# Kernel optimization log

Hardware: AMD Instinct MI355X
Metric: run time of the kernel (lower is better)

Reference implementation:

```python
import jax, jax.numpy as jnp
import numpy as np

N = 100000   # vertices
T = 128      # temporal depth
E = 1600000  # edges (avg degree 16)
K = 9        # conv kernel size
PAD = 4      # 'same' padding -> T preserved
L = 3        # number of layers


def setup_inputs() -> dict:
    key = jax.random.key(0)
    ks = jax.random.split(key, 6)
    x = jax.random.normal(ks[0], (N, T), dtype=jnp.float32)
    edge_index = jax.random.randint(ks[1], (2, E), 0, N, dtype=jnp.int32)
    conv_w = jax.random.normal(ks[2], (L, 1, 1, K), dtype=jnp.float32) * (1.0 / np.sqrt(K))
    conv_b = jax.random.normal(ks[3], (L, 1), dtype=jnp.float32) * 0.1
    W_out = jax.random.normal(ks[4], (3, N), dtype=jnp.float32) * (1.0 / np.sqrt(N))
    b_out = jax.random.normal(ks[5], (3,), dtype=jnp.float32) * 0.1
    return {"x": x, "edge_index": edge_index, "conv_w": conv_w,
            "conv_b": conv_b, "W_out": W_out, "b_out": b_out}


def _conv1d(x, w, b):
    # x: [N, T], w: [1, 1, K] (OIH), b: [1]; torch Conv1d = cross-correlation.
    y = jax.lax.conv_general_dilated(
        x[:, None, :], w, window_strides=(1,), padding=[(PAD, PAD)],
        dimension_numbers=("NCH", "OIH", "NCH"))
    return y[:, 0, :] + b  # [N, T]


def reference(x, edge_index, conv_w, conv_b, W_out, b_out):
    # add_self_loops: append (i, i) for every node
    loop = jnp.arange(N, dtype=edge_index.dtype)
    src = jnp.concatenate([edge_index[0], loop])  # message sources
    dst = jnp.concatenate([edge_index[1], loop])  # aggregation targets
    # in-degree counts (>=1 due to self loops) for mean aggregation
    cnt = jax.ops.segment_sum(jnp.ones(src.shape, jnp.float32), dst,
                              num_segments=N)[:, None]  # [N, 1]
    for i in range(L):
        h = _conv1d(x, conv_w[i], conv_b[i])                    # [N, T]
        s = jax.ops.segment_sum(h[src], dst, num_segments=N)    # scatter-sum of gathered msgs
        x = jax.nn.relu(s / cnt)                                # mean aggr + relu
    x = x.reshape(-1, N)            # [T, N] (row-major view like torch .view)
    return x @ W_out.T + b_out      # [T, 3]
```

## Files before the change

### kernel.cpp

```cpp
#include <hip/hip_runtime.h>

#define NN 100000
#define TT 128
#define EE 1600000
#define KK 9
#define NSPLIT 16
#define ZROW NN

#define BSH 9
#define BMASK 511
#define NBUCK 196
#define BCAP 10240
#define EPB 4096
#define BINB 391
#define CVTB 3125

typedef _Float16 f16;
typedef __attribute__((ext_vector_type(2))) _Float16 f16x2;
typedef __attribute__((ext_vector_type(4))) _Float16 f16x4;
typedef __attribute__((ext_vector_type(8))) _Float16 f16x8;

union HU8 { f16x8 h; int4 i; };

__global__ __launch_bounds__(1024)
void bin_cvt_kernel(const int* __restrict__ ei, int* __restrict__ gcursor,
                    unsigned int* __restrict__ binned,
                    const float4* __restrict__ x, f16x4* __restrict__ x16,
                    float* __restrict__ out,
                    int* __restrict__ zx, int* __restrict__ zyA, int* __restrict__ zyB) {
    __shared__ int hist[NBUCK];
    __shared__ int gbase[NBUCK];
    int tid = threadIdx.x;

    if (blockIdx.x >= BINB + CVTB) {
        if (tid < TT * 3) out[tid] = 0.0f;
        int k = tid - 512;
        if (k >= 0 && k < 64)        zx[k]        = 0;
        else if (k >= 64 && k < 128) zyA[k - 64]  = 0;
        else if (k >= 128 && k < 192) zyB[k - 128] = 0;
        return;
    }
    if (blockIdx.x >= BINB) {
        int i = (blockIdx.x - BINB) * 1024 + tid;
        float4 v = x[i];
        f16x4 o;
        o.x = (f16)v.x; o.y = (f16)v.y; o.z = (f16)v.z; o.w = (f16)v.w;
        x16[i] = o;
        return;
    }

    if (tid < NBUCK) hist[tid] = 0;
    __syncthreads();
    int base = blockIdx.x * EPB;
    unsigned int val[4];
    short bkt[4];
    short rank[4];
#pragma unroll
    for (int k = 0; k < 4; k++) {
        int e = base + k * 1024 + tid;
        bkt[k] = -1;
        if (e < EE) {
            int s = ei[e];
            int d = ei[EE + e];
            bkt[k] = (short)(d >> BSH);
            val[k] = ((unsigned int)(d & BMASK) << 20) | (unsigned int)s;
            rank[k] = (short)atomicAdd(&hist[bkt[k]], 1);
        }
    }
    __syncthreads();
    if (tid < NBUCK) gbase[tid] = hist[tid] ? atomicAdd(&gcursor[tid], hist[tid]) : 0;
    __syncthreads();
#pragma unroll
    for (int k = 0; k < 4; k++) {
        if (bkt[k] >= 0)
            binned[(size_t)bkt[k] * BCAP + gbase[bkt[k]] + (int)rank[k]] = val[k];
    }
}

__global__ __launch_bounds__(1024)
void bucket_csr_kernel(const unsigned int* __restrict__ binned,
                       const int* __restrict__ gcursor,
                       int* __restrict__ offsets,
                       float* __restrict__ inv_cnt,
                       int* __restrict__ col) {
    __shared__ int hist[512];
    __shared__ int cur[512];
    __shared__ int smB[256];
    __shared__ int sc[512];
    int b = blockIdx.x;
    int tid = threadIdx.x;

    if (tid < 256) smB[tid] = (tid < NBUCK) ? gcursor[tid] : 0;
    __syncthreads();
    for (int off = 1; off < 256; off <<= 1) {
        int v = 0;
        if (tid < 256 && tid >= off) v = smB[tid - off];
        __syncthreads();
        if (tid < 256) smB[tid] += v;
        __syncthreads();
    }
    int bucket_base = (b == 0) ? 0 : smB[b - 1];
    if (b == 0 && tid == 0) offsets[NN] = EE;

    int cnt = gcursor[b];
    const unsigned int* ePtr = binned + (size_t)b * BCAP;
    if (tid < 512) hist[tid] = 0;
    __syncthreads();
    for (int j = tid; j < cnt; j += 1024)
        atomicAdd(&hist[ePtr[j] >> 20], 1);
    __syncthreads();
    int d = (tid < 512) ? hist[tid] : 0;
    if (tid < 512) sc[tid] = d;
    __syncthreads();
    for (int off = 1; off < 512; off <<= 1) {
        int v = 0;
        if (tid < 512 && tid >= off) v = sc[tid - off];
        __syncthreads();
        if (tid < 512) sc[tid] += v;
        __syncthreads();
    }
    if (tid < 512) {
        int node = (b << BSH) + tid;
        int pos = bucket_base + sc[tid] - d;
        if (node < NN) {
            offsets[node] = pos;
            inv_cnt[node] = 1.0f / (1.0f + (float)d);
            cur[tid] = pos;
        }
    }
    __syncthreads();
    for (int j = tid; j < cnt; j += 1024) {
        unsigned int v = ePtr[j];
        int pos = atomicAdd(&cur[v >> 20], 1);
        col[pos] = (int)(v & 0xFFFFF);
    }
}

__global__ __launch_bounds__(128)
void fused_layer_kernel(const f16x8* __restrict__ xin,
                        const int* __restrict__ offsets,
                        const int* __restrict__ col,
                        const float* __restrict__ inv_cnt,
                        const float* __restrict__ w9,
                        const float* __restrict__ bptr,
                        f16x8* __restrict__ yout) {
    __shared__ __align__(16) f16 sb[2][144];
    int tid = threadIdx.x;
    int lane = tid & 63;
    int q = lane >> 4;
    int p = lane & 15;
    int w = tid >> 6;
    int node = __builtin_amdgcn_readfirstlane(blockIdx.x * 2 + w);

    float wr[KK];
#pragma unroll
    for (int k = 0; k < KK; k++) wr[k] = w9[k];
    float bb = bptr[0];

    if (lane < 8) {
        int k = lane;
        ((int*)&sb[w][0])[(k < 4) ? k : (64 + k)] = 0;
    }

    int lo = offsets[node], hi = offsets[node + 1];
    int cnt = hi - lo;
    int my_col = (lane < cnt) ? col[lo + lane] : ZROW;
    int jn = cnt < 64 ? cnt : 64;

    const f16 z = (f16)0;
    f16x8 acc0 = {z, z, z, z, z, z, z, z};
    f16x8 acc1 = {z, z, z, z, z, z, z, z};
    if (q == 0) acc0 = xin[(node << 4) | p];

    for (int j = 0; j < jn; j += 32) {
        int c0 = __shfl(my_col, j + q);
        int c1 = __shfl(my_col, j + 4 + q);
        int c2 = __shfl(my_col, j + 8 + q);
        int c3 = __shfl(my_col, j + 12 + q);
        int c4 = __shfl(my_col, j + 16 + q);
        int c5 = __shfl(my_col, j + 20 + q);
        int c6 = __shfl(my_col, j + 24 + q);
        int c7 = __shfl(my_col, j + 28 + q);
        f16x8 u0 = xin[(c0 << 4) | p];
        f16x8 u1 = xin[(c1 << 4) | p];
        f16x8 u2 = xin[(c2 << 4) | p];
        f16x8 u3 = xin[(c3 << 4) | p];
        f16x8 u4 = xin[(c4 << 4) | p];
        f16x8 u5 = xin[(c5 << 4) | p];
        f16x8 u6 = xin[(c6 << 4) | p];
        f16x8 u7 = xin[(c7 << 4) | p];
        acc0 += u0; acc1 += u1;
        acc0 += u2; acc1 += u3;
        acc0 += u4; acc1 += u5;
        acc0 += u6; acc1 += u7;
    }
    for (int k = 64; k < cnt; k++) {
        int c = col[lo + k];
        f16x8 v = xin[(c << 4) | p];
        if (q == 0) acc0 += v;
    }
    acc0 += acc1;

    {
        HU8 u; u.h = acc0;
        int4 o;
        o.x = __shfl_xor(u.i.x, 16); o.y = __shfl_xor(u.i.y, 16);
        o.z = __shfl_xor(u.i.z, 16); o.w = __shfl_xor(u.i.w, 16);
        HU8 w2; w2.i = o;
        acc0 += w2.h;
        u.h = acc0;
        o.x = __shfl_xor(u.i.x, 32); o.y = __shfl_xor(u.i.y, 32);
        o.z = __shfl_xor(u.i.z, 32); o.w = __shfl_xor(u.i.w, 32);
        w2.i = o;
        acc0 += w2.h;
    }

    if (q == 0) *(f16x8*)&sb[w][8 + p * 8] = acc0;

    int t0 = lane * 2;
    float A[10];
    const f16x2* sp = (const f16x2*)&sb[w][4 + t0];
#pragma unroll
    for (int i = 0; i < 5; i++) {
        f16x2 v = sp[i];
        A[2 * i]     = (float)v.x;
        A[2 * i + 1] = (float)v.y;
    }
    float ic = inv_cnt[node];
    float r0 = 0.0f, r1 = 0.0f;
#pragma unroll
    for (int k = 0; k < KK; k++) {
        r0 += wr[k] * A[k];
        r1 += wr[k] * A[k + 1];
    }
    r0 = fmaxf(r0 * ic + bb, 0.0f);
    r1 = fmaxf(r1 * ic + bb, 0.0f);
    f16x2 o;
    o.x = (f16)r0;
    o.y = (f16)r1;
    ((f16x2*)yout)[node * 64 + lane] = o;
}

__global__ void out_kernel(const f16* __restrict__ y3, const float* __restrict__ Wout,
                           const float* __restrict__ bout, float* __restrict__ out) {
    int t = blockIdx.x;
    int sp = blockIdx.y;
    int tid = threadIdx.x;
    const int per = NN / NSPLIT;
    int lo = sp * per;
    int hi = lo + per;
    float a0 = 0.0f, a1 = 0.0f, a2 = 0.0f;
    for (int n = lo + tid * 2; n < hi; n += 512) {
        f16x2 v2 = *(const f16x2*)(y3 + (size_t)t * NN + n);
        float vx = (float)v2.x, vy = (float)v2.y;
        float2 wA = *(const float2*)(Wout + n);
        float2 wB = *(const float2*)(Wout + NN + n);
        float2 wC = *(const float2*)(Wout + 2 * NN + n);
        a0 += vx * wA.x + vy * wA.y;
        a1 += vx * wB.x + vy * wB.y;
        a2 += vx * wC.x + vy * wC.y;
    }
    for (int o = 32; o > 0; o >>= 1) {
        a0 += __shfl_down(a0, o);
        a1 += __shfl_down(a1, o);
        a2 += __shfl_down(a2, o);
    }
    __shared__ float red[4][3];
    int wave = tid >> 6;
    if ((tid & 63) == 0) {
        red[wave][0] = a0;
        red[wave][1] = a1;
        red[wave][2] = a2;
    }
    __syncthreads();
    if (tid == 0) {
        float r0 = red[0][0] + red[1][0] + red[2][0] + red[3][0];
        float r1 = red[0][1] + red[1][1] + red[2][1] + red[3][1];
        float r2 = red[0][2] + red[1][2] + red[2][2] + red[3][2];
        if (sp == 0) {
            r0 += bout[0];
            r1 += bout[1];
            r2 += bout[2];
        }
        atomicAdd(&out[t * 3 + 0], r0);
        atomicAdd(&out[t * 3 + 1], r1);
        atomicAdd(&out[t * 3 + 2], r2);
    }
}

extern "C" void kernel_launch(void* const* d_in, const int* in_sizes, int n_in,
                              void* d_out, int out_size, void* d_ws, size_t ws_size,
                              hipStream_t stream) {
    const float4* x    = (const float4*)d_in[0];
    const int*    ei   = (const int*)d_in[1];
    const float*  cw   = (const float*)d_in[2];
    const float*  cb   = (const float*)d_in[3];
    const float*  Wout = (const float*)d_in[4];
    const float*  bout = (const float*)d_in[5];
    float* out = (float*)d_out;

    char* ws = (char*)d_ws;
    size_t off = 0;
    auto alloc = [&](size_t bytes) -> void* {
        void* p = ws + off;
        off += (bytes + 255) & ~(size_t)255;
        return p;
    };
    f16x8*        x16     = (f16x8*)alloc((size_t)(NN + 1) * TT * 2);
    f16x8*        yA      = (f16x8*)alloc((size_t)(NN + 1) * TT * 2);
    f16x8*        yB      = (f16x8*)alloc((size_t)(NN + 1) * TT * 2);
    unsigned int* binned  = (unsigned int*)alloc((size_t)NBUCK * BCAP * 4);
    int*          gcursor = (int*)alloc((size_t)NBUCK * 4);
    int*          offsets = (int*)alloc((size_t)(NN + 1) * 4);
    float*        inv_cnt = (float*)alloc((size_t)NN * 4);
    int*          col     = (int*)alloc((size_t)EE * 4);

    hipMemsetAsync(gcursor, 0, (size_t)NBUCK * 4, stream);
    bin_cvt_kernel<<<BINB + CVTB + 1, 1024, 0, stream>>>(
        ei, gcursor, binned, x, (f16x4*)x16, out,
        (int*)(x16 + (size_t)NN * 16), (int*)(yA + (size_t)NN * 16),
        (int*)(yB + (size_t)NN * 16));
    bucket_csr_kernel<<<NBUCK, 1024, 0, stream>>>(binned, gcursor, offsets, inv_cnt, col);

    fused_layer_kernel<<<NN / 2, 128, 0, stream>>>(x16, offsets, col, inv_cnt,
                                                   cw + 0 * KK, cb + 0, yA);
    fused_layer_kernel<<<NN / 2, 128, 0, stream>>>(yA, offsets, col, inv_cnt,
                                                   cw + 1 * KK, cb + 1, yB);
    fused_layer_kernel<<<NN / 2, 128, 0, stream>>>(yB, offsets, col, inv_cnt,
                                                   cw + 2 * KK, cb + 2, yA);

    out_kernel<<<dim3(TT, NSPLIT), 256, 0, stream>>>((const f16*)yA, Wout, bout, out);
}
```

Baseline: 321.3 us.

## Fuse output projection into final layer and reduce per-node partials deterministically

The last GNN layer now multiplies its fp32 results directly by W_out in registers and writes per-node partial sums for the (at most two) time rows each node's 128 outputs span. A small reduce kernel then sums the partials per time row without atomics. This removes the fp16 y3 write and re-read plus the separate output GEMV. In exchange it writes a partial buffer of 3.2 MB and adds extra shuffle reductions to every node's wave.

```diff
diff --git a/kernel.cpp b/kernel.cpp
--- a/kernel.cpp
+++ b/kernel.cpp
@@ -4,7 +4,6 @@
 #define TT 128
 #define EE 1600000
 #define KK 9
-#define NSPLIT 16
 #define ZROW NN
 
 #define BSH 9
@@ -26,17 +25,15 @@
 void bin_cvt_kernel(const int* __restrict__ ei, int* __restrict__ gcursor,
                     unsigned int* __restrict__ binned,
                     const float4* __restrict__ x, f16x4* __restrict__ x16,
-                    float* __restrict__ out,
                     int* __restrict__ zx, int* __restrict__ zyA, int* __restrict__ zyB) {
     __shared__ int hist[NBUCK];
     __shared__ int gbase[NBUCK];
     int tid = threadIdx.x;
 
     if (blockIdx.x >= BINB + CVTB) {
-        if (tid < TT * 3) out[tid] = 0.0f;
-        int k = tid - 512;
-        if (k >= 0 && k < 64)        zx[k]        = 0;
-        else if (k >= 64 && k < 128) zyA[k - 64]  = 0;
+        int k = tid;
+        if (k >= 0 && k < 64)         zx[k]        = 0;
+        else if (k >= 64 && k < 128)  zyA[k - 64]  = 0;
         else if (k >= 128 && k < 192) zyB[k - 128] = 0;
         return;
     }
@@ -136,30 +133,15 @@
     }
 }
 
-__global__ __launch_bounds__(128)
-void fused_layer_kernel(const f16x8* __restrict__ xin,
-                        const int* __restrict__ offsets,
-                        const int* __restrict__ col,
-                        const float* __restrict__ inv_cnt,
-                        const float* __restrict__ w9,
-                        const float* __restrict__ bptr,
-                        f16x8* __restrict__ yout) {
-    __shared__ __align__(16) f16 sb[2][144];
-    int tid = threadIdx.x;
-    int lane = tid & 63;
-    int q = lane >> 4;
-    int p = lane & 15;
-    int w = tid >> 6;
-    int node = __builtin_amdgcn_readfirstlane(blockIdx.x * 2 + w);
-
-    float wr[KK];
-#pragma unroll
-    for (int k = 0; k < KK; k++) wr[k] = w9[k];
-    float bb = bptr[0];
-
+__device__ __forceinline__ void gather_conv_node(
+    const f16x8* __restrict__ xin, const int* __restrict__ offsets,
+    const int* __restrict__ col, const float* __restrict__ inv_cnt,
+    f16* sbw, const float* wr, float bb, int node, int lane, int q, int p,
+    float& r0, float& r1)
+{
     if (lane < 8) {
         int k = lane;
-        ((int*)&sb[w][0])[(k < 4) ? k : (64 + k)] = 0;
+        ((int*)sbw)[(k < 4) ? k : (64 + k)] = 0;
     }
 
     int lo = offsets[node], hi = offsets[node + 1];
@@ -215,11 +197,11 @@
         acc0 += w2.h;
     }
 
-    if (q == 0) *(f16x8*)&sb[w][8 + p * 8] = acc0;
+    if (q == 0) *(f16x8*)&sbw[8 + p * 8] = acc0;
 
     int t0 = lane * 2;
     float A[10];
-    const f16x2* sp = (const f16x2*)&sb[w][4 + t0];
+    const f16x2* sp = (const f16x2*)&sbw[4 + t0];
 #pragma unroll
     for (int i = 0; i < 5; i++) {
         f16x2 v = sp[i];
@@ -227,7 +209,7 @@
         A[2 * i + 1] = (float)v.y;
     }
     float ic = inv_cnt[node];
-    float r0 = 0.0f, r1 = 0.0f;
+    r0 = 0.0f; r1 = 0.0f;
 #pragma unroll
     for (int k = 0; k < KK; k++) {
         r0 += wr[k] * A[k];
@@ -235,56 +217,122 @@
     }
     r0 = fmaxf(r0 * ic + bb, 0.0f);
     r1 = fmaxf(r1 * ic + bb, 0.0f);
+}
+
+__global__ __launch_bounds__(128)
+void fused_layer_kernel(const f16x8* __restrict__ xin,
+                        const int* __restrict__ offsets,
+                        const int* __restrict__ col,
+                        const float* __restrict__ inv_cnt,
+                        const float* __restrict__ w9,
+                        const float* __restrict__ bptr,
+                        f16x8* __restrict__ yout) {
+    __shared__ __align__(16) f16 sb[2][144];
+    int tid = threadIdx.x;
+    int lane = tid & 63;
+    int q = lane >> 4;
+    int p = lane & 15;
+    int w = tid >> 6;
+    int node = __builtin_amdgcn_readfirstlane(blockIdx.x * 2 + w);
+    float wr[KK];
+#pragma unroll
+    for (int k = 0; k < KK; k++) wr[k] = w9[k];
+    float r0, r1;
+    gather_conv_node(xin, offsets, col, inv_cnt, sb[w], wr, bptr[0],
+                     node, lane, q, p, r0, r1);
     f16x2 o;
     o.x = (f16)r0;
     o.y = (f16)r1;
     ((f16x2*)yout)[node * 64 + lane] = o;
 }
 
-__global__ void out_kernel(const f16* __restrict__ y3, const float* __restrict__ Wout,
-                           const float* __restrict__ bout, float* __restrict__ out) {
+__global__ __launch_bounds__(128)
+void fused_layer_head_kernel(const f16x8* __restrict__ xin,
+                             const int* __restrict__ offsets,
+                             const int* __restrict__ col,
+                             const float* __restrict__ inv_cnt,
+                             const float* __restrict__ w9,
+                             const float* __restrict__ bptr,
+                             const float* __restrict__ Wout,
+                             float4* __restrict__ partial) {
+    __shared__ __align__(16) f16 sb[2][144];
+    int tid = threadIdx.x;
+    int lane = tid & 63;
+    int q = lane >> 4;
+    int p = lane & 15;
+    int w = tid >> 6;
+    int node = __builtin_amdgcn_readfirstlane(blockIdx.x * 2 + w);
+    float wr[KK];
+#pragma unroll
+    for (int k = 0; k < KK; k++) wr[k] = w9[k];
+    float r0, r1;
+    gather_conv_node(xin, offsets, col, inv_cnt, sb[w], wr, bptr[0],
+                     node, lane, q, p, r0, r1);
+
+    int tlo  = __builtin_amdgcn_readfirstlane((node * 128) / NN);
+    int base = node * 128 - tlo * NN;
+    int n0p = base + 2 * lane;
+    int n1p = n0p + 1;
+    int hi0 = n0p >= NN;
+    int hi1 = n1p >= NN;
+    int n0 = hi0 ? n0p - NN : n0p;
+    int n1 = hi1 ? n1p - NN : n1p;
+    float aA0 = 0.f, aA1 = 0.f, aA2 = 0.f;
+    float aB0 = 0.f, aB1 = 0.f, aB2 = 0.f;
+    {
+        float c00 = r0 * Wout[0 * NN + n0], c10 = r0 * Wout[1 * NN + n0],
+              c20 = r0 * Wout[2 * NN + n0];
+        float c01 = r1 * Wout[0 * NN + n1], c11 = r1 * Wout[1 * NN + n1],
+              c21 = r1 * Wout[2 * NN + n1];
+        if (hi0) { aB0 += c00; aB1 += c10; aB2 += c20; }
+        else     { aA0 += c00; aA1 += c10; aA2 += c20; }
+        if (hi1) { aB0 += c01; aB1 += c11; aB2 += c21; }
+        else     { aA0 += c01; aA1 += c11; aA2 += c21; }
+    }
+#pragma unroll
+    for (int o = 32; o > 0; o >>= 1) {
+        aA0 += __shfl_down(aA0, o); aA1 += __shfl_down(aA1, o); aA2 += __shfl_down(aA2, o);
+        aB0 += __shfl_down(aB0, o); aB1 += __shfl_down(aB1, o); aB2 += __shfl_down(aB2, o);
+    }
+    if (lane == 0) {
+        partial[2 * node]     = make_float4(aA0, aA1, aA2, 0.0f);
+        partial[2 * node + 1] = make_float4(aB0, aB1, aB2, 0.0f);
+    }
+}
+
+__global__ __launch_bounds__(256)
+void reduce_out_kernel(const float4* __restrict__ partial,
+                       const float* __restrict__ bout,
+                       float* __restrict__ out) {
     int t = blockIdx.x;
-    int sp = blockIdx.y;
-    int tid = threadIdx.x;
-    const int per = NN / NSPLIT;
-    int lo = sp * per;
-    int hi = lo + per;
-    float a0 = 0.0f, a1 = 0.0f, a2 = 0.0f;
-    for (int n = lo + tid * 2; n < hi; n += 512) {
-        f16x2 v2 = *(const f16x2*)(y3 + (size_t)t * NN + n);
-        float vx = (float)v2.x, vy = (float)v2.y;
-        float2 wA = *(const float2*)(Wout + n);
-        float2 wB = *(const float2*)(Wout + NN + n);
-        float2 wC = *(const float2*)(Wout + 2 * NN + n);
-        a0 += vx * wA.x + vy * wA.y;
-        a1 += vx * wB.x + vy * wB.y;
-        a2 += vx * wC.x + vy * wC.y;
-    }
+    int tid = threadIdx.x;
+    int nlo = (t == 0) ? 0 : (((t - 1) * NN) + 127) >> 7;
+    int nhi = (((t + 1) * NN) - 1) >> 7;
+    if (nhi > NN - 1) nhi = NN - 1;
+    float a0 = 0.f, a1 = 0.f, a2 = 0.f;
+    for (int n = nlo + tid; n <= nhi; n += 256) {
+        int tl = (n << 7) / NN;
+        if (tl == t) {
+            float4 pa = partial[2 * n];
+            a0 += pa.x; a1 += pa.y; a2 += pa.z;
+        } else if (tl == t - 1) {
+            float4 pb = partial[2 * n + 1];
+            a0 += pb.x; a1 += pb.y; a2 += pb.z;
+        }
+    }
+#pragma unroll
     for (int o = 32; o > 0; o >>= 1) {
         a0 += __shfl_down(a0, o);
         a1 += __shfl_down(a1, o);
         a2 += __shfl_down(a2, o);
     }
     __shared__ float red[4][3];
-    int wave = tid >> 6;
-    if ((tid & 63) == 0) {
-        red[wave][0] = a0;
-        red[wave][1] = a1;
-        red[wave][2] = a2;
-    }
-    __syncthreads();
-    if (tid == 0) {
-        float r0 = red[0][0] + red[1][0] + red[2][0] + red[3][0];
-        float r1 = red[0][1] + red[1][1] + red[2][1] + red[3][1];
-        float r2 = red[0][2] + red[1][2] + red[2][2] + red[3][2];
-        if (sp == 0) {
-            r0 += bout[0];
-            r1 += bout[1];
-            r2 += bout[2];
-        }
-        atomicAdd(&out[t * 3 + 0], r0);
-        atomicAdd(&out[t * 3 + 1], r1);
-        atomicAdd(&out[t * 3 + 2], r2);
+    int wv = tid >> 6;
+    if ((tid & 63) == 0) { red[wv][0] = a0; red[wv][1] = a1; red[wv][2] = a2; }
+    __syncthreads();
+    if (tid < 3) {
+        out[t * 3 + tid] = red[0][tid] + red[1][tid] + red[2][tid] + red[3][tid]
+                         + bout[tid];
     }
 }
 
@@ -314,10 +362,11 @@
     int*          offsets = (int*)alloc((size_t)(NN + 1) * 4);
     float*        inv_cnt = (float*)alloc((size_t)NN * 4);
     int*          col     = (int*)alloc((size_t)EE * 4);
-
-    hipMemsetAsync(gcursor, 0, (size_t)NBUCK * 4, stream);
+    float4*       partial = (float4*)alloc((size_t)NN * 2 * 16);
+
+    (void)hipMemsetAsync(gcursor, 0, (size_t)NBUCK * 4, stream);
     bin_cvt_kernel<<<BINB + CVTB + 1, 1024, 0, stream>>>(
-        ei, gcursor, binned, x, (f16x4*)x16, out,
+        ei, gcursor, binned, x, (f16x4*)x16,
         (int*)(x16 + (size_t)NN * 16), (int*)(yA + (size_t)NN * 16),
         (int*)(yB + (size_t)NN * 16));
     bucket_csr_kernel<<<NBUCK, 1024, 0, stream>>>(binned, gcursor, offsets, inv_cnt, col);
@@ -326,8 +375,8 @@
                                                    cw + 0 * KK, cb + 0, yA);
     fused_layer_kernel<<<NN / 2, 128, 0, stream>>>(yA, offsets, col, inv_cnt,
                                                    cw + 1 * KK, cb + 1, yB);
-    fused_layer_kernel<<<NN / 2, 128, 0, stream>>>(yB, offsets, col, inv_cnt,
-                                                   cw + 2 * KK, cb + 2, yA);
-
-    out_kernel<<<dim3(TT, NSPLIT), 256, 0, stream>>>((const f16*)yA, Wout, bout, out);
-}
+    fused_layer_head_kernel<<<NN / 2, 128, 0, stream>>>(yB, offsets, col, inv_cnt,
+                                                        cw + 2 * KK, cb + 2, Wout,
+                                                        partial);
+    reduce_out_kernel<<<TT, 256, 0, stream>>>(partial, bout, out);
+}
```

After: 315.5 us, median of 2. Within noise of the previous version (-1.8%).
